# Performance work log

Measured on AMD Instinct MI355X. Metric: run time of the kernel, lower is better.

## Reference

```python
import jax, jax.numpy as jnp
import numpy as np
import math

B, S, H = 2, 2048, 1024
NH, HD = 16, 64  # num heads, head dim; NH*HD == H


def setup_inputs() -> dict:
    key = jax.random.key(0)
    k1, k2, k3 = jax.random.split(key, 3)
    hidden_states = jax.random.normal(k1, (B, S, H), dtype=jnp.float32)
    # causal multiplicative mask [1,1,S,S], 1.0 where attending is allowed
    mask = jnp.tril(jnp.ones((S, S), dtype=jnp.float32))[None, None]
    W_qkv = jax.random.normal(k2, (H, 3 * H), dtype=jnp.float32) * (1.0 / math.sqrt(H))
    b_qkv = jnp.zeros((3 * H,), dtype=jnp.float32)
    W_out = jax.random.normal(k3, (H, H), dtype=jnp.float32) * (1.0 / math.sqrt(H))
    b_out = jnp.zeros((H,), dtype=jnp.float32)
    return {"hidden_states": hidden_states, "mask": mask, "W_qkv": W_qkv,
            "b_qkv": b_qkv, "W_out": W_out, "b_out": b_out}


def reference(hidden_states, mask, W_qkv, b_qkv, W_out, b_out):
    b, s, h = hidden_states.shape
    # fused QKV projection then split into contiguous thirds (split_tensor_along_last_dim)
    qkv = jnp.einsum('bsh,hd->bsd', hidden_states, W_qkv) + b_qkv
    q, k, v = jnp.split(qkv, 3, axis=-1)
    # [b, s, nh*hd] -> [b, nh, s, hd]
    def to_heads(t):
        return t.reshape(b, s, NH, HD).transpose(0, 2, 1, 3)
    q, k, v = to_heads(q), to_heads(k), to_heads(v)
    q = q / jnp.sqrt(jnp.float32(HD))  # scaling_attention_score=True
    scores = jnp.einsum('bhqd,bhkd->bhqk', q, k)  # [b,nh,s,s]
    # multiplicative mask + large-negative bias trick from standard_attention
    scores = scores * mask - 10000.0 * (1.0 - mask)
    probs = jax.nn.softmax(scores, axis=-1)
    ctx = jnp.einsum('bhqk,bhkd->bhqd', probs, v)
    ctx = ctx.transpose(0, 2, 1, 3).reshape(b, s, h)  # [b, s, nh*hd]
    return jnp.einsum('bsh,hd->bsd', ctx, W_out) + b_out
```

## Files before the change

### kernel.cpp

```cpp
#include <hip/hip_runtime.h>
#include <cstdint>
#include <cstddef>

#define NHEAD 16
#define HDIM 64
#define SEQ 2048
#define BATCH 2
#define HID 1024

typedef __bf16 bf16x8 __attribute__((ext_vector_type(8)));
typedef float f32x4 __attribute__((ext_vector_type(4)));

#define AS1 __attribute__((address_space(1)))
#define AS3 __attribute__((address_space(3)))

__device__ __forceinline__ unsigned short f2bf(float f) {
    union { float f; unsigned u; } v; v.f = f;
    unsigned r = v.u + 0x7fffu + ((v.u >> 16) & 1u);
    return (unsigned short)(r >> 16);
}

__device__ __forceinline__ unsigned cvtpk_bf16(float a, float b) {
    unsigned d;
    asm("v_cvt_pk_bf16_f32 %0, %1, %2" : "=v"(d) : "v"(a), "v"(b));
    return d;
}

__global__ __launch_bounds__(256) void convert_f32_bf16(
    const float* __restrict__ in, unsigned short* __restrict__ out, int n) {
    int i = (blockIdx.x * 256 + threadIdx.x) * 8;
    if (i >= n) return;
    float4 a = *(const float4*)(in + i);
    float4 b = *(const float4*)(in + i + 4);
    uint4 o;
    o.x = (unsigned)f2bf(a.x) | ((unsigned)f2bf(a.y) << 16);
    o.y = (unsigned)f2bf(a.z) | ((unsigned)f2bf(a.w) << 16);
    o.z = (unsigned)f2bf(b.x) | ((unsigned)f2bf(b.y) << 16);
    o.w = (unsigned)f2bf(b.z) | ((unsigned)f2bf(b.w) << 16);
    *(uint4*)(out + i) = o;
}

__global__ __launch_bounds__(256) void transpose_f32_bf16(
    const float* __restrict__ in, unsigned short* __restrict__ out, int R, int C) {
    __shared__ unsigned short T[64][72];
    int t = threadIdx.x;
    int c0 = blockIdx.x * 64, r0 = blockIdx.y * 64;
    for (int p = 0; p < 4; ++p) {
        int idx = (p * 256 + t) * 4;
        int row = idx >> 6, col = idx & 63;
        float4 v = *(const float4*)(in + (size_t)(r0 + row) * C + c0 + col);
        T[row][col + 0] = f2bf(v.x);
        T[row][col + 1] = f2bf(v.y);
        T[row][col + 2] = f2bf(v.z);
        T[row][col + 3] = f2bf(v.w);
    }
    __syncthreads();
    for (int p = 0; p < 4; ++p) {
        int idx = (p * 256 + t) * 4;
        int orow = idx >> 6, ocol = idx & 63;
        ushort4 u;
        u.x = T[ocol + 0][orow];
        u.y = T[ocol + 1][orow];
        u.z = T[ocol + 2][orow];
        u.w = T[ocol + 3][orow];
        *(ushort4*)(out + (size_t)(c0 + orow) * R + r0 + ocol) = u;
    }
}

__global__ __launch_bounds__(512, 2) void gemm_qkv(
    const unsigned short* __restrict__ A, const unsigned short* __restrict__ Bt,
    const float* __restrict__ bias,
    unsigned short* __restrict__ Qb, unsigned short* __restrict__ Kb,
    unsigned short* __restrict__ Vt) {
    __shared__ unsigned short LDSu[73728];
    const int NT = 16;
    int tid = threadIdx.x;
    int wave = tid >> 6, lane = tid & 63, ln = lane & 15, quad = lane >> 4;
    int wm = wave >> 2, wn = wave & 3;
    int fid = blockIdx.y * 16 + blockIdx.x;
    int xcd = fid & 7, jj0 = fid >> 3;
    int by = (xcd & 3) * 4 + (jj0 >> 3);
    int bx = (xcd >> 2) * 8 + (jj0 & 7);
    int m0 = by * 256, n0 = bx * 192;

    int rsub = lane >> 3;
    int gs = (lane & 7) ^ rsub;

    auto stage = [&](int h) {
        if (h >= 4 * NT) return;
        int T = h >> 2, jj = h & 3;
        if (jj < 2) {
            int slot = (2 * T + jj) % 6;
            const unsigned short* src = A + (size_t)(m0 + jj * 128) * 1024 + T * 64;
#pragma unroll
            for (int p = 0; p < 2; ++p) {
                __builtin_amdgcn_global_load_lds(
                    (const AS1 void*)(src + (size_t)(p * 64 + wave * 8 + rsub) * 1024 + gs * 8),
                    (AS3 void*)&LDSu[slot * 8192 + (p * 8 + wave) * 512], 16, 0, 0);
            }
        } else {
            int slot = (2 * T + (jj - 2)) % 4;
            const unsigned short* src = Bt + (size_t)(n0 + (jj - 2) * 96) * 1024 + T * 64;
            for (int c = wave; c < 12; c += 8) {
                __builtin_amdgcn_global_load_lds(
                    (const AS1 void*)(src + (size_t)(c * 8 + rsub) * 1024 + gs * 8),
                    (AS3 void*)&LDSu[49152 + slot * 6144 + c * 512], 16, 0, 0);
            }
        }
    };

    f32x4 zero4 = {0.f, 0.f, 0.f, 0.f};
    f32x4 acc[8][3];
#pragma unroll
    for (int i = 0; i < 8; ++i)
#pragma unroll
        for (int k = 0; k < 3; ++k) acc[i][k] = zero4;

    for (int h = 0; h < 6; ++h) stage(h);
    asm volatile("s_waitcnt vmcnt(4)" ::: "memory");
    __builtin_amdgcn_s_barrier();

    for (int t = 0; t < NT; ++t) {
        int myA = (2 * t + wm) % 6;
        int myB = (2 * t + (wn >> 1)) % 4;
        const unsigned short* as = &LDSu[myA * 8192];
        const unsigned short* bs = &LDSu[49152 + myB * 6144];
        int brow = (wn & 1) * 48;
        bf16x8 bfr[3][2];
#pragma unroll
        for (int j = 0; j < 4; ++j) {
            if (j == 0) {
#pragma unroll
                for (int fn = 0; fn < 3; ++fn)
#pragma unroll
                    for (int ks = 0; ks < 2; ++ks)
                        bfr[fn][ks] = *(const bf16x8*)
                            &bs[(brow + fn * 16 + ln) * 64 + (((ks * 4 + quad) ^ (ln & 7)) * 8)];
            }
            bf16x8 af[2][2];
#pragma unroll
            for (int mi = 0; mi < 2; ++mi)
#pragma unroll
                for (int ks = 0; ks < 2; ++ks)
                    af[mi][ks] = *(const bf16x8*)
                        &as[((2 * j + mi) * 16 + ln) * 64 + (((ks * 4 + quad) ^ (ln & 7)) * 8)];
            stage(4 * t + j + 6);
            if (j == 3 && t < NT - 1) {
                if (t == NT - 2) asm volatile("s_waitcnt vmcnt(0)" ::: "memory");
                else             asm volatile("s_waitcnt vmcnt(4)" ::: "memory");
            }
            __builtin_amdgcn_s_barrier();
            asm volatile("s_waitcnt lgkmcnt(0)" ::: "memory");
            __builtin_amdgcn_sched_barrier(0);
            __builtin_amdgcn_s_setprio(1);
#pragma unroll
            for (int mi = 0; mi < 2; ++mi)
#pragma unroll
                for (int fn = 0; fn < 3; ++fn) {
                    acc[2 * j + mi][fn] = __builtin_amdgcn_mfma_f32_16x16x32_bf16(
                        af[mi][0], bfr[fn][0], acc[2 * j + mi][fn], 0, 0, 0);
                    acc[2 * j + mi][fn] = __builtin_amdgcn_mfma_f32_16x16x32_bf16(
                        af[mi][1], bfr[fn][1], acc[2 * j + mi][fn], 0, 0, 0);
                }
            __builtin_amdgcn_s_setprio(0);
            __builtin_amdgcn_s_barrier();
        }
    }

    int nbase = n0 + wn * 48;
#pragma unroll
    for (int fn = 0; fn < 3; ++fn) {
        int gn = nbase + fn * 16 + ln;
        float bv = bias[gn];
        int third = gn >> 10;
        int rem = gn & 1023;
        int h = rem >> 6, d = rem & 63;
        if (third == 2) {
#pragma unroll
            for (int fm = 0; fm < 8; ++fm) {
                int gm = m0 + wm * 128 + fm * 16 + quad * 4;
                int b = gm >> 11, s = gm & 2047;
                size_t bh = (size_t)(b * NHEAD + h);
                ushort4 u;
                u.x = f2bf(acc[fm][fn][0] + bv);
                u.y = f2bf(acc[fm][fn][1] + bv);
                u.z = f2bf(acc[fm][fn][2] + bv);
                u.w = f2bf(acc[fm][fn][3] + bv);
                *(ushort4*)&Vt[(bh * HDIM + d) * SEQ + s] = u;
            }
        } else {
            unsigned short* dst = third == 0 ? Qb : Kb;
            float scale = third == 0 ? 0.1803368801111f : 1.0f;
#pragma unroll
            for (int fm = 0; fm < 8; ++fm) {
#pragma unroll
                for (int r = 0; r < 4; ++r) {
                    int gm = m0 + wm * 128 + fm * 16 + quad * 4 + r;
                    int b = gm >> 11, s = gm & 2047;
                    size_t bh = (size_t)(b * NHEAD + h);
                    dst[(bh * SEQ + s) * HDIM + d] = f2bf((acc[fm][fn][r] + bv) * scale);
                }
            }
        }
    }
}

__global__ __launch_bounds__(256) void gemm_out(
    const unsigned short* __restrict__ A, const unsigned short* __restrict__ Bt,
    const float* __restrict__ bias, float* __restrict__ C) {
    __shared__ unsigned short As[64][32];
    __shared__ unsigned short Bs[128][32];
    int t = threadIdx.x;
    int wave = t >> 6, lane = t & 63, ln = lane & 15, quad = lane >> 4;
    int wm = wave >> 1, wn = wave & 1;
    int fid = blockIdx.y * 8 + blockIdx.x;
    int xcd = fid & 7, jj = fid >> 3;
    int by = xcd * 8 + (jj >> 3);
    int bx = jj & 7;
    int m0 = by * 64, n0 = bx * 128;
    int srow = lane >> 2, scol = (lane & 3) * 8;
    f32x4 zero4 = {0.f, 0.f, 0.f, 0.f};
    f32x4 acc[2][4];
    for (int mi = 0; mi < 2; ++mi)
        for (int ni = 0; ni < 4; ++ni) acc[mi][ni] = zero4;
    for (int kt = 0; kt < 1024; kt += 32) {
        __builtin_amdgcn_global_load_lds(
            (const AS1 void*)(A + (size_t)(m0 + wave * 16 + srow) * 1024 + kt + scol),
            (AS3 void*)&As[wave * 16][0], 16, 0, 0);
        for (int p = 0; p < 2; ++p) {
            int r0 = (wave * 2 + p) * 16 + srow;
            __builtin_amdgcn_global_load_lds(
                (const AS1 void*)(Bt + (size_t)(n0 + r0) * 1024 + kt + scol),
                (AS3 void*)&Bs[(wave * 2 + p) * 16][0], 16, 0, 0);
        }
        __syncthreads();
        bf16x8 af[2], bfr[4];
        for (int mi = 0; mi < 2; ++mi)
            af[mi] = *(const bf16x8*)&As[wm * 32 + mi * 16 + ln][quad * 8];
        for (int ni = 0; ni < 4; ++ni)
            bfr[ni] = *(const bf16x8*)&Bs[wn * 64 + ni * 16 + ln][quad * 8];
        for (int mi = 0; mi < 2; ++mi)
            for (int ni = 0; ni < 4; ++ni)
                acc[mi][ni] = __builtin_amdgcn_mfma_f32_16x16x32_bf16(
                    af[mi], bfr[ni], acc[mi][ni], 0, 0, 0);
        __syncthreads();
    }
    int nbase = n0 + wn * 64;
    for (int ni = 0; ni < 4; ++ni) {
        int gn = nbase + ni * 16 + ln;
        float bv = bias[gn];
        for (int mi = 0; mi < 2; ++mi) {
            for (int r = 0; r < 4; ++r) {
                int gm = m0 + wm * 32 + mi * 16 + quad * 4 + r;
                C[(size_t)gm * HID + gn] = acc[mi][ni][r] + bv;
            }
        }
    }
}

__global__ __launch_bounds__(256, 3) void flash_attn(
    const unsigned short* __restrict__ Qb, const unsigned short* __restrict__ Kb,
    const unsigned short* __restrict__ Vt, unsigned short* __restrict__ Ctx) {
    __shared__ unsigned short KsB[2][64][64];
    __shared__ unsigned short VsB[2][64][64];
    __shared__ unsigned short Ps[4][16][72];
    int tid = threadIdx.x;
    int wave = tid >> 6, lane = tid & 63, ln = lane & 15, quad = lane >> 4;

    int id = blockIdx.y * 32 + blockIdx.x;
    int xcd = id & 7, j = id >> 3;
    int bh = xcd * 4 + (j & 3);
    int qi = 31 - (j >> 2);
    int q0 = qi * 64;
    const size_t baseQK = (size_t)bh * SEQ * HDIM;
    const size_t baseV = (size_t)bh * HDIM * SEQ;
    int b = bh >> 4, h = bh & 15;

    int rIn = lane >> 3;
    int gsw = ((lane & 7) ^ rIn) * 8;

    bf16x8 aq0, aq1;
    {
        const unsigned short* qp =
            Qb + baseQK + (size_t)(q0 + wave * 16 + ln) * HDIM + quad * 8;
        aq0 = *(const bf16x8*)qp;
        aq1 = *(const bf16x8*)(qp + 32);
    }

    auto prefetch = [&](int kj, int bi) {
        const unsigned short* kb = Kb + baseQK + (size_t)kj * 64 * HDIM;
        const unsigned short* vb = Vt + baseV + kj * 64;
        for (int c = wave; c < 8; c += 4) {
            __builtin_amdgcn_global_load_lds(
                (const AS1 void*)(kb + (c * 8 + rIn) * HDIM + gsw),
                (AS3 void*)&KsB[bi][c * 8][0], 16, 0, 0);
            __builtin_amdgcn_global_load_lds(
                (const AS1 void*)(vb + (size_t)(c * 8 + rIn) * SEQ + gsw),
                (AS3 void*)&VsB[bi][c * 8][0], 16, 0, 0);
        }
    };

    f32x4 zero4 = {0.f, 0.f, 0.f, 0.f};
    f32x4 o[4];
    float lacc = 0.f;
    for (int i = 0; i < 4; ++i) o[i] = zero4;

    prefetch(0, 0);
    for (int t = 0; t <= qi; ++t) {
        __syncthreads();
        if (t < qi) prefetch(t + 1, (t + 1) & 1);
        int buf = t & 1;

        bf16x8 akf[2][4];
#pragma unroll
        for (int kk = 0; kk < 2; ++kk)
#pragma unroll
            for (int ni = 0; ni < 4; ++ni)
                akf[kk][ni] = *(const bf16x8*)
                    &KsB[buf][ni * 16 + ln][((kk * 4 + quad) ^ (ln & 7)) * 8];
        f32x4 s4[4];
#pragma unroll
        for (int ni = 0; ni < 4; ++ni) s4[ni] = zero4;
        __builtin_amdgcn_s_setprio(1);
#pragma unroll
        for (int kk = 0; kk < 2; ++kk) {
            bf16x8 bq = kk ? aq1 : aq0;
#pragma unroll
            for (int ni = 0; ni < 4; ++ni)
                s4[ni] = __builtin_amdgcn_mfma_f32_16x16x32_bf16(akf[kk][ni], bq, s4[ni], 0, 0, 0);
        }
        __builtin_amdgcn_s_setprio(0);

        if (t == qi) {
#pragma unroll
            for (int ni = 0; ni < 4; ++ni)
#pragma unroll
                for (int r = 0; r < 4; ++r)
                    if (ni * 16 + quad * 4 + r > wave * 16 + ln) s4[ni][r] = -1.0e38f;
        }

#pragma unroll
        for (int ni = 0; ni < 4; ++ni) {
            float e0 = __builtin_amdgcn_exp2f(s4[ni][0]);
            float e1 = __builtin_amdgcn_exp2f(s4[ni][1]);
            float e2 = __builtin_amdgcn_exp2f(s4[ni][2]);
            float e3 = __builtin_amdgcn_exp2f(s4[ni][3]);
            lacc += (e0 + e1) + (e2 + e3);
            uint2 pw;
            pw.x = cvtpk_bf16(e0, e1);
            pw.y = cvtpk_bf16(e2, e3);
            *(uint2*)&Ps[wave][ln][ni * 16 + quad * 4] = pw;
        }

        bf16x8 avf[2][4];
#pragma unroll
        for (int kk = 0; kk < 2; ++kk)
#pragma unroll
            for (int ni = 0; ni < 4; ++ni)
                avf[kk][ni] = *(const bf16x8*)
                    &VsB[buf][ni * 16 + ln][((kk * 4 + quad) ^ (ln & 7)) * 8];
        bf16x8 bp0 = *(const bf16x8*)&Ps[wave][ln][quad * 8];
        bf16x8 bp1 = *(const bf16x8*)&Ps[wave][ln][32 + quad * 8];
        __builtin_amdgcn_s_setprio(1);
#pragma unroll
        for (int ni = 0; ni < 4; ++ni)
            o[ni] = __builtin_amdgcn_mfma_f32_16x16x32_bf16(avf[0][ni], bp0, o[ni], 0, 0, 0);
#pragma unroll
        for (int ni = 0; ni < 4; ++ni)
            o[ni] = __builtin_amdgcn_mfma_f32_16x16x32_bf16(avf[1][ni], bp1, o[ni], 0, 0, 0);
        __builtin_amdgcn_s_setprio(0);
    }

    float sum = lacc;
    sum += __shfl_xor(sum, 16);
    sum += __shfl_xor(sum, 32);
    float linv = __builtin_amdgcn_rcpf(sum);
    size_t rowb = ((size_t)(b * SEQ + q0 + wave * 16 + ln)) * HID + h * 64;
#pragma unroll
    for (int ni = 0; ni < 4; ++ni) {
        ushort4 u;
        u.x = f2bf(o[ni][0] * linv);
        u.y = f2bf(o[ni][1] * linv);
        u.z = f2bf(o[ni][2] * linv);
        u.w = f2bf(o[ni][3] * linv);
        *(ushort4*)&Ctx[rowb + ni * 16 + quad * 4] = u;
    }
}

extern "C" void kernel_launch(void* const* d_in, const int* in_sizes, int n_in,
                              void* d_out, int out_size, void* d_ws, size_t ws_size,
                              hipStream_t stream) {
    const float* X = (const float*)d_in[0];
    const float* Wqkv = (const float*)d_in[2];
    const float* bqkv = (const float*)d_in[3];
    const float* Wout = (const float*)d_in[4];
    const float* bout = (const float*)d_in[5];
    float* out = (float*)d_out;

    char* ws = (char*)d_ws;
    unsigned short* Xb   = (unsigned short*)(ws + 0);
    unsigned short* W1t  = (unsigned short*)(ws + 8388608);
    unsigned short* W2t  = (unsigned short*)(ws + 14680064);
    unsigned short* Qb   = (unsigned short*)(ws + 16777216);
    unsigned short* Kb   = (unsigned short*)(ws + 25165824);
    unsigned short* Vt   = (unsigned short*)(ws + 33554432);
    unsigned short* Ctx  = (unsigned short*)(ws + 41943040);

    convert_f32_bf16<<<2048, 256, 0, stream>>>(X, Xb, 4194304);
    transpose_f32_bf16<<<dim3(48, 16), 256, 0, stream>>>(Wqkv, W1t, 1024, 3072);
    transpose_f32_bf16<<<dim3(16, 16), 256, 0, stream>>>(Wout, W2t, 1024, 1024);
    gemm_qkv<<<dim3(16, 16), 512, 0, stream>>>(Xb, W1t, bqkv, Qb, Kb, Vt);
    flash_attn<<<dim3(32, 32), 256, 0, stream>>>(Qb, Kb, Vt, Ctx);
    gemm_out<<<dim3(8, 64), 256, 0, stream>>>(Ctx, W2t, bout, out);
}
```

Measured before the change: 186.7 us.

## Halve QKV GEMM M-tile and use simple double-buffered LDS pipeline

```diff
diff --git a/kernel.cpp b/kernel.cpp
--- a/kernel.cpp
+++ b/kernel.cpp
@@ -72,99 +72,78 @@
     const float* __restrict__ bias,
     unsigned short* __restrict__ Qb, unsigned short* __restrict__ Kb,
     unsigned short* __restrict__ Vt) {
-    __shared__ unsigned short LDSu[73728];
+    __shared__ unsigned short LDSu[40960];
     const int NT = 16;
     int tid = threadIdx.x;
     int wave = tid >> 6, lane = tid & 63, ln = lane & 15, quad = lane >> 4;
     int wm = wave >> 2, wn = wave & 3;
     int fid = blockIdx.y * 16 + blockIdx.x;
-    int xcd = fid & 7, jj0 = fid >> 3;
-    int by = (xcd & 3) * 4 + (jj0 >> 3);
-    int bx = (xcd >> 2) * 8 + (jj0 & 7);
-    int m0 = by * 256, n0 = bx * 192;
+    int xcd = fid & 7, jj = fid >> 3;
+    int by = (xcd & 3) * 8 + (jj >> 3);
+    int bx = (xcd >> 2) * 8 + (jj & 7);
+    int m0 = by * 128, n0 = bx * 192;
 
     int rsub = lane >> 3;
     int gs = (lane & 7) ^ rsub;
 
-    auto stage = [&](int h) {
-        if (h >= 4 * NT) return;
-        int T = h >> 2, jj = h & 3;
-        if (jj < 2) {
-            int slot = (2 * T + jj) % 6;
-            const unsigned short* src = A + (size_t)(m0 + jj * 128) * 1024 + T * 64;
-#pragma unroll
-            for (int p = 0; p < 2; ++p) {
-                __builtin_amdgcn_global_load_lds(
-                    (const AS1 void*)(src + (size_t)(p * 64 + wave * 8 + rsub) * 1024 + gs * 8),
-                    (AS3 void*)&LDSu[slot * 8192 + (p * 8 + wave) * 512], 16, 0, 0);
-            }
-        } else {
-            int slot = (2 * T + (jj - 2)) % 4;
-            const unsigned short* src = Bt + (size_t)(n0 + (jj - 2) * 96) * 1024 + T * 64;
-            for (int c = wave; c < 12; c += 8) {
-                __builtin_amdgcn_global_load_lds(
-                    (const AS1 void*)(src + (size_t)(c * 8 + rsub) * 1024 + gs * 8),
-                    (AS3 void*)&LDSu[49152 + slot * 6144 + c * 512], 16, 0, 0);
-            }
+    auto stage = [&](int T, int bi) {
+#pragma unroll
+        for (int i = 0; i < 5; ++i) {
+            int c = wave + 8 * i;
+            const unsigned short* src;
+            int dst;
+            if (c < 16) {
+                src = A + (size_t)(m0 + c * 8 + rsub) * 1024 + T * 64 + gs * 8;
+                dst = bi * 20480 + c * 512;
+            } else {
+                src = Bt + (size_t)(n0 + (c - 16) * 8 + rsub) * 1024 + T * 64 + gs * 8;
+                dst = bi * 20480 + 8192 + (c - 16) * 512;
+            }
+            __builtin_amdgcn_global_load_lds((const AS1 void*)src,
+                                             (AS3 void*)&LDSu[dst], 16, 0, 0);
         }
     };
 
     f32x4 zero4 = {0.f, 0.f, 0.f, 0.f};
-    f32x4 acc[8][3];
-#pragma unroll
-    for (int i = 0; i < 8; ++i)
+    f32x4 acc[4][3];
+#pragma unroll
+    for (int i = 0; i < 4; ++i)
 #pragma unroll
         for (int k = 0; k < 3; ++k) acc[i][k] = zero4;
 
-    for (int h = 0; h < 6; ++h) stage(h);
-    asm volatile("s_waitcnt vmcnt(4)" ::: "memory");
-    __builtin_amdgcn_s_barrier();
+    stage(0, 0);
+    __syncthreads();
 
     for (int t = 0; t < NT; ++t) {
-        int myA = (2 * t + wm) % 6;
-        int myB = (2 * t + (wn >> 1)) % 4;
-        const unsigned short* as = &LDSu[myA * 8192];
-        const unsigned short* bs = &LDSu[49152 + myB * 6144];
-        int brow = (wn & 1) * 48;
-        bf16x8 bfr[3][2];
-#pragma unroll
-        for (int j = 0; j < 4; ++j) {
-            if (j == 0) {
-#pragma unroll
-                for (int fn = 0; fn < 3; ++fn)
-#pragma unroll
-                    for (int ks = 0; ks < 2; ++ks)
-                        bfr[fn][ks] = *(const bf16x8*)
-                            &bs[(brow + fn * 16 + ln) * 64 + (((ks * 4 + quad) ^ (ln & 7)) * 8)];
-            }
-            bf16x8 af[2][2];
-#pragma unroll
-            for (int mi = 0; mi < 2; ++mi)
-#pragma unroll
-                for (int ks = 0; ks < 2; ++ks)
-                    af[mi][ks] = *(const bf16x8*)
-                        &as[((2 * j + mi) * 16 + ln) * 64 + (((ks * 4 + quad) ^ (ln & 7)) * 8)];
-            stage(4 * t + j + 6);
-            if (j == 3 && t < NT - 1) {
-                if (t == NT - 2) asm volatile("s_waitcnt vmcnt(0)" ::: "memory");
-                else             asm volatile("s_waitcnt vmcnt(4)" ::: "memory");
-            }
-            __builtin_amdgcn_s_barrier();
-            asm volatile("s_waitcnt lgkmcnt(0)" ::: "memory");
-            __builtin_amdgcn_sched_barrier(0);
-            __builtin_amdgcn_s_setprio(1);
-#pragma unroll
-            for (int mi = 0; mi < 2; ++mi)
-#pragma unroll
-                for (int fn = 0; fn < 3; ++fn) {
-                    acc[2 * j + mi][fn] = __builtin_amdgcn_mfma_f32_16x16x32_bf16(
-                        af[mi][0], bfr[fn][0], acc[2 * j + mi][fn], 0, 0, 0);
-                    acc[2 * j + mi][fn] = __builtin_amdgcn_mfma_f32_16x16x32_bf16(
-                        af[mi][1], bfr[fn][1], acc[2 * j + mi][fn], 0, 0, 0);
-                }
-            __builtin_amdgcn_s_setprio(0);
-            __builtin_amdgcn_s_barrier();
-        }
+        int bi = t & 1;
+        const unsigned short* as = &LDSu[bi * 20480];
+        const unsigned short* bs = &LDSu[bi * 20480 + 8192];
+        if (t + 1 < NT) stage(t + 1, bi ^ 1);
+        bf16x8 bfr[3][2], af[4][2];
+#pragma unroll
+        for (int fn = 0; fn < 3; ++fn)
+#pragma unroll
+            for (int ks = 0; ks < 2; ++ks)
+                bfr[fn][ks] = *(const bf16x8*)
+                    &bs[(wn * 48 + fn * 16 + ln) * 64 + (((ks * 4 + quad) ^ (ln & 7)) * 8)];
+#pragma unroll
+        for (int fm = 0; fm < 4; ++fm)
+#pragma unroll
+            for (int ks = 0; ks < 2; ++ks)
+                af[fm][ks] = *(const bf16x8*)
+                    &as[(wm * 64 + fm * 16 + ln) * 64 + (((ks * 4 + quad) ^ (ln & 7)) * 8)];
+        __builtin_amdgcn_s_setprio(1);
+#pragma unroll
+        for (int fm = 0; fm < 4; ++fm)
+#pragma unroll
+            for (int fn = 0; fn < 3; ++fn) {
+                acc[fm][fn] = __builtin_amdgcn_mfma_f32_16x16x32_bf16(
+                    af[fm][0], bfr[fn][0], acc[fm][fn], 0, 0, 0);
+                acc[fm][fn] = __builtin_amdgcn_mfma_f32_16x16x32_bf16(
+                    af[fm][1], bfr[fn][1], acc[fm][fn], 0, 0, 0);
+            }
+        __builtin_amdgcn_s_setprio(0);
+        if (t + 1 < NT) __syncthreads();
     }
 
     int nbase = n0 + wn * 48;
@@ -177,8 +156,8 @@
         int h = rem >> 6, d = rem & 63;
         if (third == 2) {
 #pragma unroll
-            for (int fm = 0; fm < 8; ++fm) {
-                int gm = m0 + wm * 128 + fm * 16 + quad * 4;
+            for (int fm = 0; fm < 4; ++fm) {
+                int gm = m0 + wm * 64 + fm * 16 + quad * 4;
                 int b = gm >> 11, s = gm & 2047;
                 size_t bh = (size_t)(b * NHEAD + h);
                 ushort4 u;
@@ -192,10 +171,10 @@
             unsigned short* dst = third == 0 ? Qb : Kb;
             float scale = third == 0 ? 0.1803368801111f : 1.0f;
 #pragma unroll
-            for (int fm = 0; fm < 8; ++fm) {
+            for (int fm = 0; fm < 4; ++fm) {
 #pragma unroll
                 for (int r = 0; r < 4; ++r) {
-                    int gm = m0 + wm * 128 + fm * 16 + quad * 4 + r;
+                    int gm = m0 + wm * 64 + fm * 16 + quad * 4 + r;
                     int b = gm >> 11, s = gm & 2047;
                     size_t bh = (size_t)(b * NHEAD + h);
                     dst[(bh * SEQ + s) * HDIM + d] = f2bf((acc[fm][fn][r] + bv) * scale);
@@ -409,7 +388,7 @@
     convert_f32_bf16<<<2048, 256, 0, stream>>>(X, Xb, 4194304);
     transpose_f32_bf16<<<dim3(48, 16), 256, 0, stream>>>(Wqkv, W1t, 1024, 3072);
     transpose_f32_bf16<<<dim3(16, 16), 256, 0, stream>>>(Wout, W2t, 1024, 1024);
-    gemm_qkv<<<dim3(16, 16), 512, 0, stream>>>(Xb, W1t, bqkv, Qb, Kb, Vt);
+    gemm_qkv<<<dim3(16, 32), 512, 0, stream>>>(Xb, W1t, bqkv, Qb, Kb, Vt);
     flash_attn<<<dim3(32, 32), 256, 0, stream>>>(Qb, Kb, Vt, Ctx);
     gemm_out<<<dim3(8, 64), 256, 0, stream>>>(Ctx, W2t, bout, out);
 }
```

After: 181.2 us. 1.03x faster.
